# Performance work log

Measured on AMD Instinct MI355X. Metric: run time of the kernel, lower is better.

The kernel has to match this reference:

```python
import jax, jax.numpy as jnp
import numpy as np

NUM_EMBEDDINGS = 1024
EMBEDDING_DIM = 128
COMMITMENT_COST = 1.0
DECAY = 0.99
EPSILON = 1e-05
N_TOKENS = 65536


def setup_inputs() -> dict:
    key = jax.random.key(0)
    k1, k2, k3 = jax.random.split(key, 3)
    inputs = jax.random.normal(k1, (N_TOKENS, EMBEDDING_DIM), dtype=jnp.float32)
    embedding = jax.random.normal(k2, (NUM_EMBEDDINGS, EMBEDDING_DIM), dtype=jnp.float32) * 0.01
    cluster_size = jnp.ones((NUM_EMBEDDINGS,), dtype=jnp.float32)
    embed_avg = jax.random.normal(k3, (NUM_EMBEDDINGS, EMBEDDING_DIM), dtype=jnp.float32) * 0.01
    return {"inputs": inputs, "embedding": embedding,
            "cluster_size": cluster_size, "embed_avg": embed_avg}


def reference(inputs, embedding, cluster_size, embed_avg):
    # inputs: [N, D], embedding: [K, D]
    flat = inputs.reshape(-1, EMBEDDING_DIM)
    distances = (jnp.sum(flat * flat, axis=1, keepdims=True)
                 + jnp.sum(embedding * embedding, axis=1)
                 - 2.0 * flat @ embedding.T)
    idx = jnp.argmin(distances, axis=1)                       # [N]
    quantized = embedding[idx].reshape(inputs.shape)          # direct gather (same math as one-hot matmul)

    # EMA update (training path); one-hot matmuls replaced by bincount/segment_sum
    dw = jnp.zeros((NUM_EMBEDDINGS,), dtype=flat.dtype).at[idx].add(1.0)   # encodings.sum(0)
    new_cluster_size = cluster_size * DECAY + (1.0 - DECAY) * dw
    dw_embed = jax.ops.segment_sum(flat, idx, num_segments=NUM_EMBEDDINGS)  # encodings.T @ flat
    new_embed_avg = embed_avg * DECAY + (1.0 - DECAY) * dw_embed
    n = jnp.sum(new_cluster_size)
    cs = (new_cluster_size + EPSILON) / (n + NUM_EMBEDDINGS * EPSILON) * n
    new_embedding = new_embed_avg / cs[:, None]

    # losses (quantized/inputs detach semantics are identical values in fwd)
    diff2 = jnp.mean((quantized - inputs) ** 2)
    loss = diff2 + COMMITMENT_COST * diff2

    # straight-through estimator: value equals quantized
    quantized_st = inputs + jax.lax.stop_gradient(quantized - inputs)
    return (quantized_st, loss, idx, new_embedding, new_cluster_size, new_embed_avg)
```

## Files before the change

### kernel.cpp

```cpp
#include <hip/hip_runtime.h>

typedef __attribute__((ext_vector_type(8))) _Float16 half8;
typedef __attribute__((ext_vector_type(4))) float f32x4;

constexpr int NTOK = 65536;
constexpr int DIM  = 128;
constexpr int NK   = 1024;

__global__ void bprep_k(const float* __restrict__ emb, char* __restrict__ bp,
                        float* __restrict__ embT, float* __restrict__ e2s,
                        double* __restrict__ en2d, int* __restrict__ nflag) {
  int i = blockIdx.x * 256 + threadIdx.x;
  if (i == 0) *nflag = 0;
  int c = i >> 4;
  int g = i & 15;
  float4 v0 = *(const float4*)&emb[c * 128 + g * 8];
  float4 v1 = *(const float4*)&emb[c * 128 + g * 8 + 4];
  float vf[8] = {v0.x, v0.y, v0.z, v0.w, v1.x, v1.y, v1.z, v1.w};
  half8 hv;
  double pacc = 0.0;
#pragma unroll
  for (int j = 0; j < 8; j++) {
    hv[j] = (_Float16)vf[j];
    embT[(g * 8 + j) * NK + c] = vf[j];
    pacc = fma((double)vf[j], (double)vf[j], pacc);
  }
  int chunk = c >> 5, n = (c >> 4) & 1, cl = c & 15;
  int kk = g >> 2, lo4 = g & 3;
  *(half8*)(bp + chunk * 8192 + kk * 2048 + n * 1024 + (lo4 * 16 + cl) * 16) = hv;
#pragma unroll
  for (int mask = 1; mask < 16; mask <<= 1) pacc += __shfl_xor(pacc, mask);
  if (g == 0) {
    en2d[c] = pacc;
    e2s[c] = (float)(pacc * 134217728.0 + 1073741824.0);
  }
}

__global__ __launch_bounds__(128, 2)
void argmin_k(const float* __restrict__ x, const char* __restrict__ bp,
              const float* __restrict__ e2s, unsigned* __restrict__ bvh,
              unsigned* __restrict__ b2h) {
  const int t    = threadIdx.x;
  const int lane = t & 63;
  const int w    = t >> 6;
  const int l15  = lane & 15;
  const int lo4  = lane >> 4;
  const int rt   = blockIdx.x >> 1;
  const int ch   = blockIdx.x & 1;
  const int rbase = rt * 64;
  const int cbase = ch * 16;
  const int lb16 = lane * 16;

  half8 FA[4][2], FB[4][2];

#define LOADG(DST, C, KK)                                                      \
  {                                                                            \
    const char* _b = bp + ((C) * 8192 + (KK) * 2048) + lb16;                   \
    DST[0] = *(const half8*)_b;                                                \
    DST[1] = *(const half8*)(_b + 1024);                                       \
  }

#pragma unroll
  for (int kk = 0; kk < 4; kk++) LOADG(FA[kk], cbase, kk)
#pragma unroll
  for (int kk = 0; kk < 4; kk++) LOADG(FB[kk], cbase + 1, kk)

  half8 ah[2][4];
#pragma unroll
  for (int m = 0; m < 2; m++)
#pragma unroll
    for (int kk = 0; kk < 4; kk++) {
      const float* xp = &x[(rbase + w * 32 + m * 16 + l15) * 128 + kk * 32 + lo4 * 8];
      float4 v0 = *(const float4*)xp;
      float4 v1 = *(const float4*)(xp + 4);
      float vf[8] = {v0.x, v0.y, v0.z, v0.w, v1.x, v1.y, v1.z, v1.w};
      half8 av;
#pragma unroll
      for (int j = 0; j < 8; j++) av[j] = (_Float16)vf[j];
      ah[m][kk] = av;
    }

  unsigned bv[2][4], b2[2][4];
#pragma unroll
  for (int m = 0; m < 2; m++)
#pragma unroll
    for (int r = 0; r < 4; r++) { bv[m][r] = 0xFFFFFFFFu; b2[m][r] = 0xFFFFFFFFu; }

#define MFMA_PHASE(BANK, KK)                                                   \
  {                                                                            \
    acc[0][0] = __builtin_amdgcn_mfma_f32_16x16x32_f16(ah[0][KK], BANK[KK][0], acc[0][0], 0, 0, 0); \
    acc[1][0] = __builtin_amdgcn_mfma_f32_16x16x32_f16(ah[1][KK], BANK[KK][0], acc[1][0], 0, 0, 0); \
    acc[0][1] = __builtin_amdgcn_mfma_f32_16x16x32_f16(ah[0][KK], BANK[KK][1], acc[0][1], 0, 0, 0); \
    acc[1][1] = __builtin_amdgcn_mfma_f32_16x16x32_f16(ah[1][KK], BANK[KK][1], acc[1][1], 0, 0, 0); \
  }

#define KEY_EPI(C)                                                             \
  {                                                                            \
    _Pragma("unroll")                                                          \
    for (int n = 0; n < 2; n++) {                                              \
      unsigned col = (unsigned)((C) * 32 + n * 16 + l15);                      \
      float e2v = n ? e2b : e2a;                                               \
      _Pragma("unroll")                                                        \
      for (int m = 0; m < 2; m++)                                              \
        _Pragma("unroll")                                                      \
        for (int r = 0; r < 4; r++) {                                          \
          float ks = fmaf(acc[m][n][r], -268435456.0f, e2v);                   \
          unsigned key = ((unsigned)ks & 0xFFFFFC00u) | col;                   \
          unsigned old = bv[m][r];                                             \
          bv[m][r] = min(old, key);                                            \
          b2[m][r] = min(b2[m][r], max(old, key));                             \
        }                                                                      \
    }                                                                          \
  }

  for (int i = 0; i < 16; i += 2) {
    const int cg = cbase + i;
    {
      float e2a = e2s[cg * 32 + l15];
      float e2b = e2s[cg * 32 + 16 + l15];
      f32x4 acc[2][2];
#pragma unroll
      for (int m = 0; m < 2; m++)
#pragma unroll
        for (int n = 0; n < 2; n++) acc[m][n] = (f32x4)(0.0f);
#pragma unroll
      for (int kk = 0; kk < 4; kk++) {
        MFMA_PHASE(FA, kk)
        if (i + 2 < 16) LOADG(FA[kk], cg + 2, kk)
      }
      KEY_EPI(cg)
    }
    {
      float e2a = e2s[(cg + 1) * 32 + l15];
      float e2b = e2s[(cg + 1) * 32 + 16 + l15];
      f32x4 acc[2][2];
#pragma unroll
      for (int m = 0; m < 2; m++)
#pragma unroll
        for (int n = 0; n < 2; n++) acc[m][n] = (f32x4)(0.0f);
#pragma unroll
      for (int kk = 0; kk < 4; kk++) {
        MFMA_PHASE(FB, kk)
        if (i + 3 < 16) LOADG(FB[kk], cg + 3, kk)
      }
      KEY_EPI(cg + 1)
    }
  }
#undef LOADG
#undef MFMA_PHASE
#undef KEY_EPI

#pragma unroll
  for (int m = 0; m < 2; m++)
#pragma unroll
    for (int r = 0; r < 4; r++) {
      unsigned v = bv[m][r], v2 = b2[m][r];
      for (int mask = 1; mask < 16; mask <<= 1) {
        unsigned ov = __shfl_xor(v, mask);
        unsigned o2 = __shfl_xor(v2, mask);
        v2 = min(min(v2, o2), max(v, ov));
        v  = min(v, ov);
      }
      if (l15 == 0) {
        int row = rbase + w * 32 + m * 16 + lo4 * 4 + r;
        bvh[ch * NTOK + row] = v;
        b2h[ch * NTOK + row] = v2;
      }
    }
}

__global__ __launch_bounds__(1024)
void merge_k(const unsigned* __restrict__ bvh, const unsigned* __restrict__ b2h,
             int* __restrict__ idx_arr, float* __restrict__ out_idx,
             int* __restrict__ nflag, int* __restrict__ flags,
             unsigned* __restrict__ bcount) {
  __shared__ unsigned bins[NK];
  int t = threadIdx.x;
  bins[t] = 0u;
  __syncthreads();
  int row = blockIdx.x * 1024 + t;
  unsigned va = bvh[row], vb = bvh[NTOK + row];
  unsigned v2 = min(min(b2h[row], b2h[NTOK + row]), max(va, vb));
  unsigned v  = min(va, vb);
  int ii = (int)(v & 1023u);
  idx_arr[row] = ii;
  out_idx[row] = (float)ii;
  atomicAdd(&bins[ii], 1u);
  if ((v2 >> 10) - (v >> 10) < 79u) {
    int p = atomicAdd(nflag, 1); flags[p] = row;
  }
  __syncthreads();
  bcount[blockIdx.x * NK + t] = bins[t];
}

__global__ __launch_bounds__(256)
void fb_k(const float* __restrict__ x, const float* __restrict__ embT,
          const double* __restrict__ en2d, const int* __restrict__ nflag,
          const int* __restrict__ flags, int* __restrict__ idx_arr,
          float* __restrict__ out_idx, unsigned* __restrict__ bcount) {
  int n = *nflag;
  __shared__ double xsh[4][DIM];
  __shared__ double sv[256];
  __shared__ int    si[256];
  int t = threadIdx.x;
  double n0 = en2d[t * 4 + 0], n1 = en2d[t * 4 + 1];
  double n2 = en2d[t * 4 + 2], n3 = en2d[t * 4 + 3];
  for (int base = blockIdx.x * 4; base < n; base += gridDim.x * 4) {
    int nb = min(4, n - base);
    __syncthreads();
    for (int u = t; u < nb * DIM; u += 256) {
      int j = u >> 7, d = u & 127;
      xsh[j][d] = (double)x[flags[base + j] * DIM + d];
    }
    __syncthreads();
    double xe[4][4];
#pragma unroll
    for (int j = 0; j < 4; j++)
#pragma unroll
      for (int q = 0; q < 4; q++) xe[j][q] = 0.0;
    for (int d = 0; d < DIM; d++) {
      float4 v = *(const float4*)&embT[d * NK + t * 4];
      double e0 = (double)v.x, e1 = (double)v.y, e2 = (double)v.z, e3 = (double)v.w;
#pragma unroll
      for (int j = 0; j < 4; j++) {
        double xd = xsh[j][d];
        xe[j][0] = fma(e0, xd, xe[j][0]);
        xe[j][1] = fma(e1, xd, xe[j][1]);
        xe[j][2] = fma(e2, xd, xe[j][2]);
        xe[j][3] = fma(e3, xd, xe[j][3]);
      }
    }
#pragma unroll
    for (int j = 0; j < 4; j++) {
      double s0 = n0 - 2.0 * xe[j][0];
      double s1 = n1 - 2.0 * xe[j][1];
      double s2 = n2 - 2.0 * xe[j][2];
      double s3 = n3 - 2.0 * xe[j][3];
      double bvv = s0; int bii = t * 4;
      if (s1 < bvv) { bvv = s1; bii = t * 4 + 1; }
      if (s2 < bvv) { bvv = s2; bii = t * 4 + 2; }
      if (s3 < bvv) { bvv = s3; bii = t * 4 + 3; }
      sv[t] = bvv; si[t] = bii;
      __syncthreads();
      for (int sh = 128; sh > 0; sh >>= 1) {
        if (t < sh) {
          double ov = sv[t + sh]; int oi = si[t + sh];
          if (ov < sv[t] || (ov == sv[t] && oi < si[t])) { sv[t] = ov; si[t] = oi; }
        }
        __syncthreads();
      }
      if (t == 0 && j < nb) {
        int row = flags[base + j];
        int nw = si[0];
        int old = idx_arr[row];
        if (nw != old) {
          idx_arr[row] = nw;
          out_idx[row] = (float)nw;
          int b = row >> 10;
          atomicSub(&bcount[b * NK + old], 1u);
          atomicAdd(&bcount[b * NK + nw], 1u);
        }
      }
      __syncthreads();
    }
  }
}

__global__ void scan_k(unsigned* __restrict__ bcount, unsigned* __restrict__ icounts,
                       unsigned* __restrict__ offsets, const float* __restrict__ cs,
                       float* __restrict__ out_ncs, float* __restrict__ csk) {
  __shared__ unsigned sc[NK];
  __shared__ float sf[NK];
  int t = threadIdx.x;
  unsigned tot = 0;
#pragma unroll 8
  for (int b = 0; b < 64; b++) tot += bcount[b * NK + t];
  icounts[t] = tot;
  sc[t] = tot;
  __syncthreads();
  for (int off = 1; off < NK; off <<= 1) {
    unsigned v = (t >= off) ? sc[t - off] : 0u;
    __syncthreads();
    sc[t] += v;
    __syncthreads();
  }
  unsigned excl = sc[t] - tot;
  offsets[t] = excl;
  unsigned run = excl;
#pragma unroll 8
  for (int b = 0; b < 64; b++) {
    unsigned c = bcount[b * NK + t];
    bcount[b * NK + t] = run;
    run += c;
  }
  float c0 = cs[t];
  float ncs = c0 * 0.99f + 0.01f * (float)tot;
  out_ncs[t] = ncs;
  sf[t] = c0;
  __syncthreads();
  for (int s = 512; s > 0; s >>= 1) {
    if (t < s) sf[t] += sf[t + s];
    __syncthreads();
  }
  float n = 0.99f * sf[0] + 655.36f;
  csk[t] = (ncs + 1e-5f) / (n + 1024.0f * 1e-5f) * n;
}

__global__ __launch_bounds__(1024)
void scatter_k(const int* __restrict__ idx, const unsigned* __restrict__ bstart,
               int* __restrict__ order) {
  __shared__ unsigned cur[NK];
  int t = threadIdx.x;
  cur[t] = bstart[blockIdx.x * NK + t];
  __syncthreads();
  int r = blockIdx.x * 1024 + t;
  unsigned p = atomicAdd(&cur[idx[r]], 1u);
  order[p] = r;
}

__global__ __launch_bounds__(512)
void fgather_k(const float* __restrict__ x, const float* __restrict__ emb,
               const unsigned* __restrict__ offsets, const unsigned* __restrict__ icounts,
               const int* __restrict__ order, float* __restrict__ out_q,
               float* __restrict__ dwsum2, float* __restrict__ partial2) {
  __shared__ int ids[1024];
  int k = blockIdx.x >> 1, half = blockIdx.x & 1;
  int t = threadIdx.x;
  int d = t & 127, h = t >> 7;
  unsigned cnt = icounts[k];
  unsigned chl = cnt >> 1;
  unsigned s = offsets[k] + (half ? chl : 0u);
  unsigned myc = half ? (cnt - chl) : chl;
  for (unsigned j = t; j < myc && j < 1024u; j += 512) ids[j] = order[s + j];
  __syncthreads();
  float e = emb[k * DIM + d];
  float acc = 0.f, ls = 0.f;
#pragma unroll 4
  for (unsigned j = h; j < myc; j += 4) {
    int row = (j < 1024u) ? ids[j] : order[s + j];
    float xv = x[row * DIM + d];
    out_q[row * DIM + d] = e;
    acc += xv;
    float dd = e - xv;
    ls += dd * dd;
  }
  __shared__ float sa[512], sl[512];
  sa[t] = acc; sl[t] = ls;
  __syncthreads();
  if (t < 128) dwsum2[(half * NK + k) * DIM + t] = sa[t] + sa[t + 128] + sa[t + 256] + sa[t + 384];
  for (int sh = 256; sh > 0; sh >>= 1) {
    if (t < sh) sl[t] += sl[t + sh];
    __syncthreads();
  }
  if (t == 0) partial2[blockIdx.x] = sl[0];
}

__global__ void emb_k(const float* __restrict__ embed_avg, const float* __restrict__ dwsum2,
                      const float* __restrict__ csk, const float* __restrict__ partial2,
                      float* __restrict__ out_nemb, float* __restrict__ out_nea,
                      float* __restrict__ out_loss) {
  if (blockIdx.x == 0) {
    __shared__ float red[256];
    int t = threadIdx.x;
    float v = 0.f;
#pragma unroll
    for (int i = 0; i < 8; i++) v += partial2[t + 256 * i];
    red[t] = v;
    __syncthreads();
    for (int sh = 128; sh > 0; sh >>= 1) {
      if (t < sh) red[t] += red[t + sh];
      __syncthreads();
    }
    if (t == 0) out_loss[0] = 2.0f * red[0] / 8388608.0f;
    return;
  }
  int i = (blockIdx.x - 1) * 256 + threadIdx.x;
  float dw = dwsum2[i] + dwsum2[NK * DIM + i];
  float na = embed_avg[i] * 0.99f + 0.01f * dw;
  out_nea[i] = na;
  out_nemb[i] = na / csk[i >> 7];
}

extern "C" void kernel_launch(void* const* d_in, const int* in_sizes, int n_in,
                              void* d_out, int out_size, void* d_ws, size_t ws_size,
                              hipStream_t stream) {
  const float* x   = (const float*)d_in[0];
  const float* emb = (const float*)d_in[1];
  const float* cs  = (const float*)d_in[2];
  const float* ea  = (const float*)d_in[3];

  float* out      = (float*)d_out;
  float* out_q    = out;
  float* out_loss = out + 8388608;
  float* out_idx  = out + 8388609;
  float* out_nemb = out + 8454145;
  float* out_ncs  = out + 8585217;
  float* out_nea  = out + 8586241;

  float* W        = (float*)d_ws;
  float* e2s      = W;
  double* en2d    = (double*)(W + 1024);
  char*  bpack    = (char*)(W + 3072);
  float* embT     = W + 72704;
  unsigned* bcount = (unsigned*)(W + 203776);
  unsigned* icounts = (unsigned*)(W + 269312);
  unsigned* offsets = (unsigned*)(W + 270336);
  float* csk      = W + 271360;
  int*   nflag    = (int*)(W + 272384);
  int*   flags    = (int*)(W + 272400);
  int*   idx_arr  = (int*)(W + 337936);
  int*   order    = (int*)(W + 403472);
  unsigned* bvh   = (unsigned*)(W + 469008);
  unsigned* b2h   = (unsigned*)(W + 600080);
  float* dwsum2   = W + 731152;
  float* partial2 = W + 993296;

  bprep_k<<<64, 256, 0, stream>>>(emb, bpack, embT, e2s, en2d, nflag);
  argmin_k<<<2048, 128, 0, stream>>>(x, bpack, e2s, bvh, b2h);
  merge_k<<<64, 1024, 0, stream>>>(bvh, b2h, idx_arr, out_idx, nflag, flags, bcount);
  fb_k<<<256, 256, 0, stream>>>(x, embT, en2d, nflag, flags, idx_arr, out_idx, bcount);
  scan_k<<<1, 1024, 0, stream>>>(bcount, icounts, offsets, cs, out_ncs, csk);
  scatter_k<<<64, 1024, 0, stream>>>(idx_arr, bcount, order);
  fgather_k<<<2048, 512, 0, stream>>>(x, emb, offsets, icounts, order, out_q, dwsum2, partial2);
  emb_k<<<513, 256, 0, stream>>>(ea, dwsum2, csk, partial2, out_nemb, out_nea, out_loss);
}
```

Before: 103.6 us.

## Fuse column-half merge into argmin kernel via LDS and move histogram after fallback

```diff
diff --git a/kernel.cpp b/kernel.cpp
--- a/kernel.cpp
+++ b/kernel.cpp
@@ -38,17 +38,17 @@
 
 __global__ __launch_bounds__(128, 2)
 void argmin_k(const float* __restrict__ x, const char* __restrict__ bp,
-              const float* __restrict__ e2s, unsigned* __restrict__ bvh,
-              unsigned* __restrict__ b2h) {
+              const float* __restrict__ e2s, int* __restrict__ idx_arr,
+              float* __restrict__ out_idx, int* __restrict__ nflag,
+              int* __restrict__ flags) {
+  __shared__ unsigned kvs[2][32], k2s[2][32];
   const int t    = threadIdx.x;
   const int lane = t & 63;
   const int w    = t >> 6;
   const int l15  = lane & 15;
   const int lo4  = lane >> 4;
-  const int rt   = blockIdx.x >> 1;
-  const int ch   = blockIdx.x & 1;
-  const int rbase = rt * 64;
-  const int cbase = ch * 16;
+  const int rbase = blockIdx.x * 32;
+  const int cbase = w * 16;
   const int lb16 = lane * 16;
 
   half8 FA[4][2], FB[4][2];
@@ -70,7 +70,7 @@
   for (int m = 0; m < 2; m++)
 #pragma unroll
     for (int kk = 0; kk < 4; kk++) {
-      const float* xp = &x[(rbase + w * 32 + m * 16 + l15) * 128 + kk * 32 + lo4 * 8];
+      const float* xp = &x[(rbase + m * 16 + l15) * 128 + kk * 32 + lo4 * 8];
       float4 v0 = *(const float4*)xp;
       float4 v1 = *(const float4*)(xp + 4);
       float vf[8] = {v0.x, v0.y, v0.z, v0.w, v1.x, v1.y, v1.z, v1.w};
@@ -162,42 +162,32 @@
         v  = min(v, ov);
       }
       if (l15 == 0) {
-        int row = rbase + w * 32 + m * 16 + lo4 * 4 + r;
-        bvh[ch * NTOK + row] = v;
-        b2h[ch * NTOK + row] = v2;
-      }
-    }
-}
-
-__global__ __launch_bounds__(1024)
-void merge_k(const unsigned* __restrict__ bvh, const unsigned* __restrict__ b2h,
-             int* __restrict__ idx_arr, float* __restrict__ out_idx,
-             int* __restrict__ nflag, int* __restrict__ flags,
-             unsigned* __restrict__ bcount) {
-  __shared__ unsigned bins[NK];
-  int t = threadIdx.x;
-  bins[t] = 0u;
-  __syncthreads();
-  int row = blockIdx.x * 1024 + t;
-  unsigned va = bvh[row], vb = bvh[NTOK + row];
-  unsigned v2 = min(min(b2h[row], b2h[NTOK + row]), max(va, vb));
-  unsigned v  = min(va, vb);
-  int ii = (int)(v & 1023u);
-  idx_arr[row] = ii;
-  out_idx[row] = (float)ii;
-  atomicAdd(&bins[ii], 1u);
-  if ((v2 >> 10) - (v >> 10) < 79u) {
-    int p = atomicAdd(nflag, 1); flags[p] = row;
-  }
-  __syncthreads();
-  bcount[blockIdx.x * NK + t] = bins[t];
+        int lr = m * 16 + lo4 * 4 + r;
+        kvs[w][lr] = v;
+        k2s[w][lr] = v2;
+      }
+    }
+  __syncthreads();
+
+  if (t < 32) {
+    unsigned va = kvs[0][t], vb = kvs[1][t];
+    unsigned v2 = min(min(k2s[0][t], k2s[1][t]), max(va, vb));
+    unsigned v  = min(va, vb);
+    int row = rbase + t;
+    int ii = (int)(v & 1023u);
+    idx_arr[row] = ii;
+    out_idx[row] = (float)ii;
+    if ((v2 >> 10) - (v >> 10) < 79u) {
+      int p = atomicAdd(nflag, 1); flags[p] = row;
+    }
+  }
 }
 
 __global__ __launch_bounds__(256)
 void fb_k(const float* __restrict__ x, const float* __restrict__ embT,
           const double* __restrict__ en2d, const int* __restrict__ nflag,
           const int* __restrict__ flags, int* __restrict__ idx_arr,
-          float* __restrict__ out_idx, unsigned* __restrict__ bcount) {
+          float* __restrict__ out_idx) {
   int n = *nflag;
   __shared__ double xsh[4][DIM];
   __shared__ double sv[256];
@@ -251,19 +241,24 @@
       }
       if (t == 0 && j < nb) {
         int row = flags[base + j];
-        int nw = si[0];
-        int old = idx_arr[row];
-        if (nw != old) {
-          idx_arr[row] = nw;
-          out_idx[row] = (float)nw;
-          int b = row >> 10;
-          atomicSub(&bcount[b * NK + old], 1u);
-          atomicAdd(&bcount[b * NK + nw], 1u);
-        }
+        idx_arr[row] = si[0];
+        out_idx[row] = (float)si[0];
       }
       __syncthreads();
     }
   }
+}
+
+__global__ void histb_k(const int* __restrict__ idx, unsigned* __restrict__ bcount) {
+  __shared__ unsigned bins[NK];
+  int t = threadIdx.x;
+  for (int b = t; b < NK; b += 256) bins[b] = 0u;
+  __syncthreads();
+#pragma unroll
+  for (int j = 0; j < 4; j++)
+    atomicAdd(&bins[idx[blockIdx.x * 1024 + j * 256 + t]], 1u);
+  __syncthreads();
+  for (int b = t; b < NK; b += 256) bcount[blockIdx.x * NK + b] = bins[b];
 }
 
 __global__ void scan_k(unsigned* __restrict__ bcount, unsigned* __restrict__ icounts,
@@ -410,15 +405,13 @@
   int*   flags    = (int*)(W + 272400);
   int*   idx_arr  = (int*)(W + 337936);
   int*   order    = (int*)(W + 403472);
-  unsigned* bvh   = (unsigned*)(W + 469008);
-  unsigned* b2h   = (unsigned*)(W + 600080);
-  float* dwsum2   = W + 731152;
-  float* partial2 = W + 993296;
+  float* dwsum2   = W + 469008;
+  float* partial2 = W + 731152;
 
   bprep_k<<<64, 256, 0, stream>>>(emb, bpack, embT, e2s, en2d, nflag);
-  argmin_k<<<2048, 128, 0, stream>>>(x, bpack, e2s, bvh, b2h);
-  merge_k<<<64, 1024, 0, stream>>>(bvh, b2h, idx_arr, out_idx, nflag, flags, bcount);
-  fb_k<<<256, 256, 0, stream>>>(x, embT, en2d, nflag, flags, idx_arr, out_idx, bcount);
+  argmin_k<<<2048, 128, 0, stream>>>(x, bpack, e2s, idx_arr, out_idx, nflag, flags);
+  fb_k<<<256, 256, 0, stream>>>(x, embT, en2d, nflag, flags, idx_arr, out_idx);
+  histb_k<<<64, 256, 0, stream>>>(idx_arr, bcount);
   scan_k<<<1, 1024, 0, stream>>>(bcount, icounts, offsets, cs, out_ncs, csk);
   scatter_k<<<64, 1024, 0, stream>>>(idx_arr, bcount, order);
   fgather_k<<<2048, 512, 0, stream>>>(x, emb, offsets, icounts, order, out_q, dwsum2, partial2);
```

Result: no change. 102.0 us (-1.5%).
